# Optimization experiments

Measured on AMD Instinct MI355X. Metric: run time of the kernel, lower is better.

Reference implementation:

```python
import jax, jax.numpy as jnp
import numpy as np

B, IN_SEQ, TGT_SEQ = 128, 50, 25
IN_SIZE, OUT_SIZE, RNN = 128, 128, 2048


def setup_inputs() -> dict:
    key = jax.random.key(0)
    ks = jax.random.split(key, 10)
    s_in = 1.0 / np.sqrt(IN_SIZE)
    s_out = 1.0 / np.sqrt(OUT_SIZE)
    s_rnn = 1.0 / np.sqrt(RNN)
    return {
        "encoder_inputs": jax.random.normal(ks[0], (B, IN_SEQ, IN_SIZE), jnp.float32),
        "decoder_inputs": jax.random.normal(ks[1], (B, TGT_SEQ, IN_SIZE), jnp.float32),
        "fc1_w": jax.random.uniform(ks[2], (OUT_SIZE, IN_SIZE), jnp.float32, -s_in, s_in),
        "fc1_b": jax.random.uniform(ks[3], (OUT_SIZE,), jnp.float32, -s_in, s_in),
        "w_ih": jax.random.uniform(ks[4], (3 * RNN, OUT_SIZE), jnp.float32, -s_rnn, s_rnn),
        "w_hh": jax.random.uniform(ks[5], (3 * RNN, RNN), jnp.float32, -s_rnn, s_rnn),
        "b_ih": jax.random.uniform(ks[6], (3 * RNN,), jnp.float32, -s_rnn, s_rnn),
        "b_hh": jax.random.uniform(ks[7], (3 * RNN,), jnp.float32, -s_rnn, s_rnn),
        "fc2_w": jax.random.uniform(ks[8], (OUT_SIZE, RNN), jnp.float32, -s_rnn, s_rnn),
        "fc2_b": jax.random.uniform(ks[9], (OUT_SIZE,), jnp.float32, -s_rnn, s_rnn),
    }


def _gru_cell(x, h, w_ih, w_hh, b_ih, b_hh):
    # PyTorch GRUCell: gates ordered (r, z, n)
    gi = x @ w_ih.T + b_ih            # [B, 3R]
    gh = h @ w_hh.T + b_hh            # [B, 3R]
    i_r, i_z, i_n = jnp.split(gi, 3, axis=-1)
    h_r, h_z, h_n = jnp.split(gh, 3, axis=-1)
    r = jax.nn.sigmoid(i_r + h_r)
    z = jax.nn.sigmoid(i_z + h_z)
    n = jnp.tanh(i_n + r * h_n)
    return (1.0 - z) * n + z * h


def reference(encoder_inputs, decoder_inputs, fc1_w, fc1_b, w_ih, w_hh, b_ih, b_hh, fc2_w, fc2_b):
    # Eval mode: F.dropout(training=False) is identity.
    enc = encoder_inputs @ fc1_w.T + fc1_b              # [B, S_in, OUT]
    enc_t = jnp.transpose(enc, (1, 0, 2))               # time-major [S_in, B, OUT]
    h0 = jnp.zeros((encoder_inputs.shape[0], RNN), enc.dtype)

    def enc_step(state, x):
        return _gru_cell(x, state, w_ih, w_hh, b_ih, b_hh), None

    state, _ = jax.lax.scan(enc_step, h0, enc_t[:-1])   # input_seq - 1 steps

    def dec_step(carry, _):
        state, inp = carry
        inp = jax.lax.stop_gradient(inp)                # inp.detach()
        state = _gru_cell(inp, state, w_ih, w_hh, b_ih, b_hh)
        out = inp + state @ fc2_w.T + fc2_b             # residual decoder
        return (state, out), out

    _, outs = jax.lax.scan(dec_step, (state, enc_t[-1]), None, length=TGT_SEQ)
    return jnp.transpose(outs, (1, 0, 2))               # [B, TGT_SEQ, OUT]
```

## Files before the change

kernel.cpp:

```cpp
#include <hip/hip_runtime.h>
#include <limits.h>

constexpr int kB   = 128;
constexpr int kSin = 50;
constexpr int kT   = 25;
constexpr int kD   = 128;
constexpr int kR   = 2048;
constexpr int kNB  = 256;
constexpr int kNT  = 512;
constexpr int kRing = 8;

typedef __bf16 bf16x8 __attribute__((ext_vector_type(8)));
typedef float  f32x4  __attribute__((ext_vector_type(4)));
typedef unsigned short u16;
typedef unsigned long long u64;

__device__ __forceinline__ float bf2f(u16 u){ union{unsigned i; float f;}x; x.i=((unsigned)u)<<16; return x.f; }
__device__ __forceinline__ u16 f2bf(float f){ union{float f; unsigned i;}x; x.f=f; return (u16)((x.i + 0x7FFFu + ((x.i>>16)&1u))>>16); }
__device__ __forceinline__ float sigm(float x){ return 1.f/(1.f+__expf(-x)); }

__device__ __forceinline__ void stg32(unsigned* p, unsigned v){
    __hip_atomic_store(p, v, __ATOMIC_RELAXED, __HIP_MEMORY_SCOPE_AGENT);
}
__device__ __forceinline__ void stg64(u64* p, u64 v){
    __hip_atomic_store(p, v, __ATOMIC_RELAXED, __HIP_MEMORY_SCOPE_AGENT);
}
__device__ __forceinline__ unsigned ald32(const void* p){
    return __hip_atomic_load((const unsigned*)p, __ATOMIC_RELAXED, __HIP_MEMORY_SCOPE_AGENT);
}
__device__ __forceinline__ u64 ald64(const void* p){
    return __hip_atomic_load((const u64*)p, __ATOMIC_RELAXED, __HIP_MEMORY_SCOPE_AGENT);
}
__device__ __forceinline__ bf16x8 ald128bf(const u16* p){
    union{ u64 q[2]; bf16x8 v; } t;
    t.q[0] = ald64(p);
    t.q[1] = ald64(p + 4);
    return t.v;
}
__device__ __forceinline__ float aldf(const float* p){
    union{ unsigned u; float f; } t; t.u = ald32(p); return t.f;
}

__device__ __forceinline__ bf16x8 pack8(float4 a, float4 b){
    union{ bf16x8 v; u16 u[8]; } t;
    t.u[0]=f2bf(a.x); t.u[1]=f2bf(a.y); t.u[2]=f2bf(a.z); t.u[3]=f2bf(a.w);
    t.u[4]=f2bf(b.x); t.u[5]=f2bf(b.y); t.u[6]=f2bf(b.z); t.u[7]=f2bf(b.w);
    return t.v;
}

__device__ __forceinline__ int pollflag(int* flags, int idx, int iter){
    if ((iter & 31) == 31) return atomicMax(&flags[idx*16], INT_MIN);
    return (int)ald32(&flags[idx*16]);
}
__device__ __forceinline__ void wait16(int* flags, int k, int base){
    const int lane = threadIdx.x & 63;
    for (int iter = 0;; ++iter){
        bool ok = true;
        if (lane < 16) ok = (pollflag(flags, base + lane, iter) >= k);
        if (__ballot(ok) == ~0ull) return;
        __builtin_amdgcn_s_sleep(1);
    }
}
__device__ __forceinline__ void wait128(int* flags, int k, int base){
    const int lane = threadIdx.x & 63;
    for (int iter = 0;; ++iter){
        bool ok = true;
#pragma unroll
        for (int j = 0; j < 2; ++j)
            ok &= (pollflag(flags, base + lane*2 + j, iter) >= k);
        if (__ballot(ok) == ~0ull) return;
        __builtin_amdgcn_s_sleep(1);
    }
}
__device__ __forceinline__ void arrive(int* flags, int k){
    __syncthreads();
    if (threadIdx.x == 0) atomicMax(&flags[blockIdx.x*16], k);
}

__device__ __forceinline__ void gbar(int* flags, int k, int base, int perlane)
{
    __syncthreads();
    const int tid = threadIdx.x;
    if (tid == 0) atomicMax(&flags[blockIdx.x*16], k);
    if (tid < 64) {
        int iter = 0;
        for (;;) {
            bool ok = true;
            for (int j = 0; j < perlane; ++j) {
                const int idx = base + tid*perlane + j;
                int v;
                if ((iter & 31) == 31) v = atomicMax(&flags[idx*16], INT_MIN);
                else                   v = (int)ald32(&flags[idx*16]);
                ok &= (v >= k);
            }
            if (__ballot(ok) == ~0ull) break;
            ++iter;
            __builtin_amdgcn_s_sleep(1);
        }
    }
    __syncthreads();
}

__device__ __forceinline__ void cvt_f32_bf16(const float* __restrict__ s, u16* __restrict__ d,
                                             int n4, int gtid, int gstride)
{
    for (int i = gtid; i < n4; i += gstride) {
        float4 v = ((const float4*)s)[i];
        u64 pk = (u64)f2bf(v.x) | ((u64)f2bf(v.y)<<16) | ((u64)f2bf(v.z)<<32) | ((u64)f2bf(v.w)<<48);
        stg64((u64*)d + i, pk);
    }
}

template<int NT, int NACC>
__device__ __forceinline__ void small_gemm(
    const u16* __restrict__ Am, int alda,
    const u16* __restrict__ Bp, int bldb,
    f32x4 (&acc)[NACC], u16* pool)
{
    const int tid=threadIdx.x, lane=tid&63, wv=tid>>6, g=wv>>2, mt=wv&3, ar=lane&15, aq=lane>>4;
    u16* sA = pool;
    u16* sB = pool + 8704;
    { int q=tid,     r=q>>4, c=q&15; *(uint4*)&sA[r*136+c*8] = *(const uint4*)(Am + r*alda + c*8); }
    { int q=tid+512, r=q>>4, c=q&15; *(uint4*)&sA[r*136+c*8] = *(const uint4*)(Am + r*alda + c*8); }
    for (int q=tid; q<NT*256; q+=kNT){
        int r=q>>4, c=q&15;
        *(uint4*)&sB[r*136+c*8] = *(const uint4*)(Bp + (size_t)r*bldb + c*8);
    }
    __syncthreads();
#pragma unroll
    for (int jt=0; jt<NT; ++jt){
        if ((jt&1) != g) continue;
#pragma unroll
        for (int kk=0; kk<4; ++kk){
            bf16x8 a = *(const bf16x8*)&sA[(mt*16+ar)*136 + kk*32 + aq*8];
            bf16x8 b = *(const bf16x8*)&sB[(jt*16+ar)*136 + kk*32 + aq*8];
            acc[jt>>1] = __builtin_amdgcn_mfma_f32_16x16x32_bf16(a,b,acc[jt>>1],0,0,0);
        }
    }
    __syncthreads();
}

__device__ __forceinline__ void gru_phase_flag(
    const u16* __restrict__ hcur, u16* __restrict__ hnxt,
    const u16* __restrict__ xb,
    const bf16x8 (&wB)[3][8], const bf16x8 (&wI)[3],
    const float4 b4, float (&hprev)[4],
    int wgc, int mrow0, u16* smem, u16* sH,
    int* flags, int hk, int xk, int fbase, bool dofence)
{
    const int tid=threadIdx.x, lane=tid&63, w=tid>>6, ar=lane&15, aq=lane>>4;
    const f32x4 zz = {0.f,0.f,0.f,0.f};
    f32x4 acc[3][4] = {{zz,zz,zz,zz},{zz,zz,zz,zz},{zz,zz,zz,zz}};
    f32x4 xn[4] = {zz,zz,zz,zz};

    if (dofence) __builtin_amdgcn_fence(__ATOMIC_ACQUIRE, "agent");

    if (hk) wait16(flags, hk, fbase + 16*w);

#pragma unroll
    for (int mt=0; mt<4; ++mt){
        const int row = mrow0 + mt*16 + ar;
        bf16x8 af[8];
#pragma unroll
        for (int c=0; c<8; ++c){
            const int s = 16*w + 2*c + (aq>>1);
            af[c] = *(const bf16x8*)(hcur + (((s*128 + row)<<4) + (aq&1)*8));
        }
#pragma unroll
        for (int c=0; c<8; ++c){
            acc[0][mt] = __builtin_amdgcn_mfma_f32_16x16x32_bf16(af[c], wB[0][c], acc[0][mt],0,0,0);
            acc[1][mt] = __builtin_amdgcn_mfma_f32_16x16x32_bf16(af[c], wB[1][c], acc[1][mt],0,0,0);
            acc[2][mt] = __builtin_amdgcn_mfma_f32_16x16x32_bf16(af[c], wB[2][c], acc[2][mt],0,0,0);
        }
    }
    if (w < 4){
        if (xk) wait128(flags, xk, fbase);
#pragma unroll
        for (int mt=0; mt<4; ++mt){
            bf16x8 ax = *(const bf16x8*)(xb + (mrow0+mt*16+ar)*kD + 32*w + aq*8);
            acc[0][mt] = __builtin_amdgcn_mfma_f32_16x16x32_bf16(ax, wI[0], acc[0][mt],0,0,0);
            acc[1][mt] = __builtin_amdgcn_mfma_f32_16x16x32_bf16(ax, wI[1], acc[1][mt],0,0,0);
            xn[mt]     = __builtin_amdgcn_mfma_f32_16x16x32_bf16(ax, wI[2], xn[mt],0,0,0);
        }
    }
    float* red = (float*)smem;
#define RCELL(wp,g4,mt) (red + (((((wp)*4+(g4))*4+(mt))*64 + lane)<<2))
    if (w >= 4){
#pragma unroll
        for (int g=0; g<3; ++g)
#pragma unroll
            for (int mt=0; mt<4; ++mt)
                *(f32x4*)RCELL(w-4, g, mt) = acc[g][mt];
    }
    __syncthreads();
    if (w < 4){
#pragma unroll
        for (int g=0; g<3; ++g)
#pragma unroll
            for (int mt=0; mt<4; ++mt)
                acc[g][mt] += *(f32x4*)RCELL(w, g, mt);
#pragma unroll
        for (int g=0; g<3; ++g)
#pragma unroll
            for (int mt=0; mt<4; ++mt)
                *(f32x4*)RCELL(w, g, mt) = acc[g][mt];
#pragma unroll
        for (int mt=0; mt<4; ++mt)
            *(f32x4*)RCELL(w, 3, mt) = xn[mt];
    }
    __syncthreads();
    if (tid < 256){
        const int mt = tid>>6, ls = tid&63, aqs = ls>>4, ars = ls&15;
        f32x4 R=zz, Z=zz, NH=zz, NX=zz;
#pragma unroll
        for (int wp=0; wp<4; ++wp){
            R  += *(f32x4*)(red + ((((wp*4+0)*4+mt)*64 + ls)<<2));
            Z  += *(f32x4*)(red + ((((wp*4+1)*4+mt)*64 + ls)<<2));
            NH += *(f32x4*)(red + ((((wp*4+2)*4+mt)*64 + ls)<<2));
            NX += *(f32x4*)(red + ((((wp*4+3)*4+mt)*64 + ls)<<2));
        }
#pragma unroll
        for (int rr=0; rr<4; ++rr){
            const int m = mrow0 + mt*16 + aqs*4 + rr;
            float r_ = sigm(R[rr] + b4.x);
            float z_ = sigm(Z[rr] + b4.y);
            float n_ = tanhf(NX[rr] + b4.z + r_*(NH[rr] + b4.w));
            float hn = (1.f-z_)*n_ + z_*hprev[rr];
            hprev[rr] = hn;
            u16 hb = f2bf(hn);
            sH[(mt*16 + aqs*4 + rr)*16 + ars] = hb;
            unsigned other = (unsigned)__shfl_xor((int)(unsigned)hb, 1);
            if (!(ars&1))
                stg32((unsigned*)(hnxt + ((wgc*128+m)<<4) + ars), (unsigned)hb | (other<<16));
        }
    }
#undef RCELL
    __syncthreads();
}

__device__ __forceinline__ void fc2_partial(
    const u16* __restrict__ sH, const bf16x8 (&wF2)[4],
    int wgc, int mh, float* __restrict__ part)
{
    const int tid=threadIdx.x, lane=tid&63, w=tid>>6, ar=lane&15, aq=lane>>4;
    const int mt = w&3, nh = w>>2;
    bf16x8 a;
    if (aq < 2) a = *(const bf16x8*)&sH[(mt*16+ar)*16 + aq*8];
    else {
#pragma unroll
        for (int i=0;i<8;++i) a[i] = (__bf16)0.f;
    }
    const f32x4 zz = {0.f,0.f,0.f,0.f};
    f32x4 acc[4] = {zz,zz,zz,zz};
#pragma unroll
    for (int j=0;j<4;++j)
        acc[j] = __builtin_amdgcn_mfma_f32_16x16x32_bf16(a, wF2[j], acc[j],0,0,0);
#pragma unroll
    for (int j=0;j<4;++j){
        const int col = (nh*4+j)*16 + ar;
#pragma unroll
        for (int rr=0;rr<4;++rr){
            const int row = mt*16 + aq*4 + rr;
            stg32((unsigned*)(part + ((((size_t)mh*64+row)*128 + wgc)*128 + col)),
                  __float_as_uint(acc[j][rr]));
        }
    }
}

__global__ __launch_bounds__(kNT, 2) void seq2seq_kernel(
    const void* __restrict__ enc_in_raw, const void* __restrict__ fc1_w_raw,
    const void* __restrict__ fc1_b_raw,  const void* __restrict__ w_ih_raw,
    const void* __restrict__ w_hh_raw,   const void* __restrict__ b_ih_raw,
    const void* __restrict__ b_hh_raw,   const void* __restrict__ fc2_w_raw,
    const void* __restrict__ fc2_b_raw,
    void* __restrict__ out_raw,
    u16* __restrict__ enc_act,
    u16* __restrict__ h_b16,
    u16* __restrict__ inp_b16,
    float* __restrict__ inp_f32,
    float* __restrict__ encF,
    float* __restrict__ bias,
    float* __restrict__ part,
    int* flags,
    u16* __restrict__ cv_encx, u16* __restrict__ cv_fc2, u16* __restrict__ cv_fc1)
{
    __shared__ __align__(16) u16 smem[33792];
    __shared__ int sflag;
    u16* sH = smem + 32768;
    const int wg = blockIdx.x, tid = threadIdx.x;
    const int wgc = wg & 127, mrow0 = (wg >> 7) * 64;
    const int lane = tid & 63, wv = tid >> 6, ar = lane & 15, aq = lane >> 4;
    const int gtid = wg * kNT + tid, gstride = kNB * kNT;
    const int dom = (wg >> 7) * 128;
    const size_t HS = (size_t)kB*kR;

    {
        const u16* p = (const u16*)enc_in_raw;
        int found = 0;
        for (int i = tid; i < 16384; i += kNT) found |= ((p[i] & 0x7F80) == 0x7F80) ? 1 : 0;
        if (tid == 0) sflag = 0;
        __syncthreads();
        if (found) sflag = 1;
        __syncthreads();
    }
    const bool F32 = (sflag != 0);

    bf16x8 wB[3][8];
    bf16x8 wI[3];
    {
        const int w4 = wv & 3;
        if (F32){
            const float* Wh = (const float*)w_hh_raw;
            const float* Wi = (const float*)w_ih_raw;
#pragma unroll
            for (int g=0; g<3; ++g)
#pragma unroll
                for (int c=0; c<8; ++c){
                    size_t o = (size_t)(g*kR + wgc*16 + ar)*kR + 256*wv + 32*c + aq*8;
                    wB[g][c] = pack8(*(const float4*)(Wh+o), *(const float4*)(Wh+o+4));
                }
#pragma unroll
            for (int g=0; g<3; ++g){
                size_t o = (size_t)(g*kR + wgc*16 + ar)*kD + 32*w4 + aq*8;
                wI[g] = pack8(*(const float4*)(Wi+o), *(const float4*)(Wi+o+4));
            }
        } else {
            const u16* Wh = (const u16*)w_hh_raw;
            const u16* Wi = (const u16*)w_ih_raw;
#pragma unroll
            for (int g=0; g<3; ++g)
#pragma unroll
                for (int c=0; c<8; ++c)
                    wB[g][c] = *(const bf16x8*)(Wh + (size_t)(g*kR + wgc*16 + ar)*kR + 256*wv + 32*c + aq*8);
#pragma unroll
            for (int g=0; g<3; ++g)
                wI[g] = *(const bf16x8*)(Wi + (size_t)(g*kR + wgc*16 + ar)*kD + 32*w4 + aq*8);
        }
    }

    if (F32) {
        cvt_f32_bf16((const float*)fc2_w_raw, cv_fc2,  (kD*kR)/4,       gtid, gstride);
        cvt_f32_bf16((const float*)fc1_w_raw, cv_fc1,  (kD*kD)/4,       gtid, gstride);
        cvt_f32_bf16((const float*)enc_in_raw,cv_encx, (kB*kSin*kD)/4,  gtid, gstride);
        for (int i = gtid; i < 3*kR; i += gstride) {
            stg32((unsigned*)&bias[i],        __float_as_uint(((const float*)b_ih_raw)[i]));
            stg32((unsigned*)&bias[3*kR + i], __float_as_uint(((const float*)b_hh_raw)[i]));
        }
        for (int i = gtid; i < kD; i += gstride) {
            stg32((unsigned*)&bias[6*kR + i],      __float_as_uint(((const float*)fc1_b_raw)[i]));
            stg32((unsigned*)&bias[6*kR + kD + i], __float_as_uint(((const float*)fc2_b_raw)[i]));
        }
    } else {
        for (int i = gtid; i < 3*kR; i += gstride) {
            stg32((unsigned*)&bias[i],        __float_as_uint(bf2f(((const u16*)b_ih_raw)[i])));
            stg32((unsigned*)&bias[3*kR + i], __float_as_uint(bf2f(((const u16*)b_hh_raw)[i])));
        }
        for (int i = gtid; i < kD; i += gstride) {
            stg32((unsigned*)&bias[6*kR + i],      __float_as_uint(bf2f(((const u16*)fc1_b_raw)[i])));
            stg32((unsigned*)&bias[6*kR + kD + i], __float_as_uint(bf2f(((const u16*)fc2_b_raw)[i])));
        }
    }
    for (int i = gtid; i < (int)((kB*kR)/2); i += gstride) stg32((unsigned*)h_b16 + i, 0u);
    gbar(flags, 1, 0, 4);

    const u16* ENCX = F32 ? cv_encx : (const u16*)enc_in_raw;
    const u16* WF2  = F32 ? cv_fc2  : (const u16*)fc2_w_raw;
    const u16* WF1  = F32 ? cv_fc1  : (const u16*)fc1_w_raw;

    float4 b4;
    {
        const int hc = wgc*16 + ar;
        b4.x = aldf(&bias[hc])      + aldf(&bias[3*kR+hc]);
        b4.y = aldf(&bias[kR+hc])   + aldf(&bias[4*kR+hc]);
        b4.z = aldf(&bias[2*kR+hc]);
        b4.w = aldf(&bias[5*kR+hc]);
    }
    bf16x8 wF2[4];
    {
        const int nh = wv>>2;
#pragma unroll
        for (int j=0;j<4;++j){
            if (aq < 2)
                wF2[j] = ald128bf(WF2 + (size_t)((nh*4+j)*16+ar)*kR + wgc*16 + aq*8);
            else {
#pragma unroll
                for (int i=0;i<8;++i) wF2[j][i] = (__bf16)0.f;
            }
        }
    }
    const float fc2b = aldf(&bias[6*kR + kD + (wg&1)*64 + (tid&63)]);
    float hprev[4] = {0.f, 0.f, 0.f, 0.f};

    if (wgc < kSin) {
        const int g = wv>>2, mt = wv&3;
        const f32x4 zz = {0.f,0.f,0.f,0.f};
        f32x4 ae[4] = {zz,zz,zz,zz};
        small_gemm<8,4>(ENCX + ((size_t)mrow0*kSin + wgc)*kD, kSin*kD, WF1, kD, ae, smem);
#pragma unroll
        for (int jt=0; jt<8; ++jt){
            if ((jt&1) != g) continue;
            int col = jt*16 + ar;
            float fb = aldf(&bias[6*kR + col]);
#pragma unroll
            for (int rr=0; rr<4; ++rr){
                int m = mrow0 + mt*16 + aq*4 + rr;
                float v = ae[jt>>1][rr] + fb;
                u16 hb = f2bf(v);
                unsigned other = (unsigned)__shfl_xor((int)(unsigned)hb, 1);
                if (!(ar&1))
                    stg32((unsigned*)(enc_act + ((size_t)wgc*kB + m)*kD + col),
                          (unsigned)hb | (other<<16));
                if (wgc == kSin-1)
                    stg32((unsigned*)(encF + (size_t)m*kD + col), __float_as_uint(v));
            }
        }
    }
    gbar(flags, 2, dom, 2);

    for (int t = 0; t < kSin-1; ++t) {
        gru_phase_flag(h_b16 + (size_t)(t & 7)*HS, h_b16 + (size_t)((t+1) & 7)*HS,
                       enc_act + (size_t)t*kB*kD, wB, wI, b4, hprev, wgc, mrow0, smem, sH,
                       flags, (t==0 ? 0 : t+2), 0, dom,
                       (t > 0) && ((t & 7) == 0));
        arrive(flags, t+3);
    }

    const u16*   ib  = enc_act + (size_t)(kSin-1)*kB*kD;
    const float* ifp = encF;
    const int mh = wg >> 7;
    for (int d = 0; d < kT; ++d) {
        const int g = 49 + d;
        gru_phase_flag(h_b16 + (size_t)(g & 7)*HS, h_b16 + (size_t)((g+1) & 7)*HS,
                       ib, wB, wI, b4, hprev, wgc, mrow0, smem, sH,
                       flags, (d==0 ? 51 : 50+2*d), (d==0 ? 0 : 51+2*d), dom,
                       (g & 7) == 0);
        fc2_partial(sH, wF2, wgc, mh, part);
        arrive(flags, 52+2*d);

        u16*   nib = inp_b16 + (size_t)(d & 7)*kB*kD;
        float* nif = inp_f32 + (size_t)(d & 7)*kB*kD;
        wait128(flags, 52+2*d, dom);
        {
            const int row = wg >> 1, ch = wg & 1;
            const int mh2 = row >> 6, rl = row & 63;
            const float* pr = part + (size_t)((mh2*64 + rl)*128)*128;
            const int cl = tid & 63, sg = tid >> 6;
            float s = 0.f;
#pragma unroll
            for (int j=0;j<16;++j) s += aldf(&pr[(size_t)(sg*16+j)*128 + ch*64 + cl]);
            float* red2 = (float*)smem;
            red2[sg*64 + cl] = s;
            __syncthreads();
            if (tid < 64){
                float t2 = 0.f;
#pragma unroll
                for (int g2=0; g2<8; ++g2) t2 += red2[g2*64 + tid];
                const int colg = ch*64 + tid;
                const float o = t2 + fc2b + ifp[(size_t)row*kD + colg];
                const size_t ob = ((size_t)row*kT + d)*kD + colg;
                if (F32) ((float*)out_raw)[ob] = o;
                else     ((u16*)out_raw)[ob]   = f2bf(o);
                stg32((unsigned*)(nif + (size_t)row*kD + colg), __float_as_uint(o));
                u16 hb = f2bf(o);
                unsigned other = (unsigned)__shfl_xor((int)(unsigned)hb, 1);
                if (!(tid&1))
                    stg32((unsigned*)(nib + (size_t)row*kD + colg), (unsigned)hb | (other<<16));
            }
        }
        arrive(flags, 53+2*d);
        ib = nib; ifp = nif;
    }
}

extern "C" void kernel_launch(void* const* d_in, const int* in_sizes, int n_in,
                              void* d_out, int out_size, void* d_ws, size_t ws_size,
                              hipStream_t stream)
{
    size_t off = 0;
    char* ws = (char*)d_ws;
    auto alloc = [&](size_t bytes) -> char* {
        char* p = ws + off;
        off = (off + bytes + 255) & ~(size_t)255;
        return p;
    };
    u16*   enc_act = (u16*)alloc((size_t)kSin*kB*kD*2);
    u16*   h_b16   = (u16*)alloc((size_t)kRing*kB*kR*2);
    u16*   inp_b16 = (u16*)alloc((size_t)kRing*kB*kD*2);
    float* inp_f32 = (float*)alloc((size_t)kRing*kB*kD*4);
    float* encF    = (float*)alloc((size_t)kB*kD*4);
    float* bias    = (float*)alloc((size_t)(6*kR + 2*kD)*4);
    float* part    = (float*)alloc((size_t)2*64*128*128*4);
    int*   flags   = (int*)alloc((size_t)kNB*16*4);
    u16*   cv_encx = (u16*)alloc((size_t)kB*kSin*kD*2);
    u16*   cv_fc2  = (u16*)alloc((size_t)kD*kR*2);
    u16*   cv_fc1  = (u16*)alloc((size_t)kD*kD*2);
    (void)ws_size; (void)in_sizes; (void)n_in; (void)out_size;

    seq2seq_kernel<<<dim3(kNB), dim3(kNT), 0, stream>>>(
        d_in[0], d_in[2], d_in[3], d_in[4], d_in[5], d_in[6], d_in[7], d_in[8], d_in[9],
        d_out,
        enc_act, h_b16, inp_b16, inp_f32, encF, bias, part, flags,
        cv_encx, cv_fc2, cv_fc1);
}
```

Before: 1.531 ms.

## Software-pipeline h-fragment loads in GRU phase, reload fc2 weights per step

Restructures the recurrent GEMM so the h fragments for two M-tiles are double-buffered: the loads for the next tile are issued while the MFMAs for the current one run, and the x-input loads are hoisted ahead of the h MFMAs. The fc2 weight fragments are no longer held in registers for the whole kernel; they are reloaded from global memory on each decoder step, which frees VGPRs for the double buffers. tanhf is replaced by an exp-based fast tanh. The shared-memory array is enlarged but not visibly used, and the per-step weight reloads add memory traffic on the decoder path.

```diff
diff --git a/kernel.cpp b/kernel.cpp
--- a/kernel.cpp
+++ b/kernel.cpp
@@ -18,6 +18,7 @@
 __device__ __forceinline__ float bf2f(u16 u){ union{unsigned i; float f;}x; x.i=((unsigned)u)<<16; return x.f; }
 __device__ __forceinline__ u16 f2bf(float f){ union{float f; unsigned i;}x; x.f=f; return (u16)((x.i + 0x7FFFu + ((x.i>>16)&1u))>>16); }
 __device__ __forceinline__ float sigm(float x){ return 1.f/(1.f+__expf(-x)); }
+__device__ __forceinline__ float tanhf_fast(float x){ return 1.f - 2.f/(__expf(2.f*x)+1.f); }
 
 __device__ __forceinline__ void stg32(unsigned* p, unsigned v){
     __hip_atomic_store(p, v, __ATOMIC_RELAXED, __HIP_MEMORY_SCOPE_AGENT);
@@ -27,15 +28,6 @@
 }
 __device__ __forceinline__ unsigned ald32(const void* p){
     return __hip_atomic_load((const unsigned*)p, __ATOMIC_RELAXED, __HIP_MEMORY_SCOPE_AGENT);
-}
-__device__ __forceinline__ u64 ald64(const void* p){
-    return __hip_atomic_load((const u64*)p, __ATOMIC_RELAXED, __HIP_MEMORY_SCOPE_AGENT);
-}
-__device__ __forceinline__ bf16x8 ald128bf(const u16* p){
-    union{ u64 q[2]; bf16x8 v; } t;
-    t.q[0] = ald64(p);
-    t.q[1] = ald64(p + 4);
-    return t.v;
 }
 __device__ __forceinline__ float aldf(const float* p){
     union{ unsigned u; float f; } t; t.u = ald32(p); return t.f;
@@ -140,6 +132,14 @@
     __syncthreads();
 }
 
+#define MT_MFMA(MT, BUF)                                                            \
+    _Pragma("unroll")                                                               \
+    for (int c=0; c<8; ++c){                                                        \
+        acc[0][MT] = __builtin_amdgcn_mfma_f32_16x16x32_bf16(BUF[c], wB[0][c], acc[0][MT],0,0,0); \
+        acc[1][MT] = __builtin_amdgcn_mfma_f32_16x16x32_bf16(BUF[c], wB[1][c], acc[1][MT],0,0,0); \
+        acc[2][MT] = __builtin_amdgcn_mfma_f32_16x16x32_bf16(BUF[c], wB[2][c], acc[2][MT],0,0,0); \
+    }
+
 __device__ __forceinline__ void gru_phase_flag(
     const u16* __restrict__ hcur, u16* __restrict__ hnxt,
     const u16* __restrict__ xb,
@@ -157,32 +157,39 @@
 
     if (hk) wait16(flags, hk, fbase + 16*w);
 
-#pragma unroll
-    for (int mt=0; mt<4; ++mt){
-        const int row = mrow0 + mt*16 + ar;
-        bf16x8 af[8];
-#pragma unroll
-        for (int c=0; c<8; ++c){
-            const int s = 16*w + 2*c + (aq>>1);
-            af[c] = *(const bf16x8*)(hcur + (((s*128 + row)<<4) + (aq&1)*8));
-        }
-#pragma unroll
-        for (int c=0; c<8; ++c){
-            acc[0][mt] = __builtin_amdgcn_mfma_f32_16x16x32_bf16(af[c], wB[0][c], acc[0][mt],0,0,0);
-            acc[1][mt] = __builtin_amdgcn_mfma_f32_16x16x32_bf16(af[c], wB[1][c], acc[1][mt],0,0,0);
-            acc[2][mt] = __builtin_amdgcn_mfma_f32_16x16x32_bf16(af[c], wB[2][c], acc[2][mt],0,0,0);
-        }
-    }
+#define HPTR(MT,C) ((const bf16x8*)(hcur + ((((16*w + 2*(C) + (aq>>1))*128 + mrow0 + (MT)*16 + ar)<<4) + (aq&1)*8)))
+    bf16x8 af0[8], af1[8];
+#pragma unroll
+    for (int c=0;c<8;++c) af0[c] = *HPTR(0,c);
+#pragma unroll
+    for (int c=0;c<8;++c) af1[c] = *HPTR(1,c);
+
+    bf16x8 ax[4];
     if (w < 4){
         if (xk) wait128(flags, xk, fbase);
 #pragma unroll
+        for (int mt=0; mt<4; ++mt)
+            ax[mt] = *(const bf16x8*)(xb + (mrow0+mt*16+ar)*kD + 32*w + aq*8);
+    }
+
+    MT_MFMA(0, af0)
+#pragma unroll
+    for (int c=0;c<8;++c) af0[c] = *HPTR(2,c);
+    MT_MFMA(1, af1)
+    if (w < 4){
+#pragma unroll
         for (int mt=0; mt<4; ++mt){
-            bf16x8 ax = *(const bf16x8*)(xb + (mrow0+mt*16+ar)*kD + 32*w + aq*8);
-            acc[0][mt] = __builtin_amdgcn_mfma_f32_16x16x32_bf16(ax, wI[0], acc[0][mt],0,0,0);
-            acc[1][mt] = __builtin_amdgcn_mfma_f32_16x16x32_bf16(ax, wI[1], acc[1][mt],0,0,0);
-            xn[mt]     = __builtin_amdgcn_mfma_f32_16x16x32_bf16(ax, wI[2], xn[mt],0,0,0);
-        }
-    }
+            acc[0][mt] = __builtin_amdgcn_mfma_f32_16x16x32_bf16(ax[mt], wI[0], acc[0][mt],0,0,0);
+            acc[1][mt] = __builtin_amdgcn_mfma_f32_16x16x32_bf16(ax[mt], wI[1], acc[1][mt],0,0,0);
+            xn[mt]     = __builtin_amdgcn_mfma_f32_16x16x32_bf16(ax[mt], wI[2], xn[mt],0,0,0);
+        }
+    }
+#pragma unroll
+    for (int c=0;c<8;++c) af1[c] = *HPTR(3,c);
+    MT_MFMA(2, af0)
+    MT_MFMA(3, af1)
+#undef HPTR
+
     float* red = (float*)smem;
 #define RCELL(wp,g4,mt) (red + (((((wp)*4+(g4))*4+(mt))*64 + lane)<<2))
     if (w >= 4){
@@ -224,7 +231,7 @@
             const int m = mrow0 + mt*16 + aqs*4 + rr;
             float r_ = sigm(R[rr] + b4.x);
             float z_ = sigm(Z[rr] + b4.y);
-            float n_ = tanhf(NX[rr] + b4.z + r_*(NH[rr] + b4.w));
+            float n_ = tanhf_fast(NX[rr] + b4.z + r_*(NH[rr] + b4.w));
             float hn = (1.f-z_)*n_ + z_*hprev[rr];
             hprev[rr] = hn;
             u16 hb = f2bf(hn);
@@ -239,22 +246,30 @@
 }
 
 __device__ __forceinline__ void fc2_partial(
-    const u16* __restrict__ sH, const bf16x8 (&wF2)[4],
+    const u16* __restrict__ sH, const u16* __restrict__ WF2,
     int wgc, int mh, float* __restrict__ part)
 {
     const int tid=threadIdx.x, lane=tid&63, w=tid>>6, ar=lane&15, aq=lane>>4;
     const int mt = w&3, nh = w>>2;
-    bf16x8 a;
-    if (aq < 2) a = *(const bf16x8*)&sH[(mt*16+ar)*16 + aq*8];
-    else {
+    bf16x8 a, wj[4];
+    if (aq < 2){
+        a = *(const bf16x8*)&sH[(mt*16+ar)*16 + aq*8];
+#pragma unroll
+        for (int j=0;j<4;++j)
+            wj[j] = *(const bf16x8*)(WF2 + (size_t)((nh*4+j)*16+ar)*kR + wgc*16 + aq*8);
+    } else {
 #pragma unroll
         for (int i=0;i<8;++i) a[i] = (__bf16)0.f;
+#pragma unroll
+        for (int j=0;j<4;++j)
+#pragma unroll
+            for (int i=0;i<8;++i) wj[j][i] = (__bf16)0.f;
     }
     const f32x4 zz = {0.f,0.f,0.f,0.f};
     f32x4 acc[4] = {zz,zz,zz,zz};
 #pragma unroll
     for (int j=0;j<4;++j)
-        acc[j] = __builtin_amdgcn_mfma_f32_16x16x32_bf16(a, wF2[j], acc[j],0,0,0);
+        acc[j] = __builtin_amdgcn_mfma_f32_16x16x32_bf16(a, wj[j], acc[j],0,0,0);
 #pragma unroll
     for (int j=0;j<4;++j){
         const int col = (nh*4+j)*16 + ar;
@@ -284,7 +299,7 @@
     int* flags,
     u16* __restrict__ cv_encx, u16* __restrict__ cv_fc2, u16* __restrict__ cv_fc1)
 {
-    __shared__ __align__(16) u16 smem[33792];
+    __shared__ __align__(16) u16 smem[43008];
     __shared__ int sflag;
     u16* sH = smem + 32768;
     const int wg = blockIdx.x, tid = threadIdx.x;
@@ -374,19 +389,6 @@
         b4.y = aldf(&bias[kR+hc])   + aldf(&bias[4*kR+hc]);
         b4.z = aldf(&bias[2*kR+hc]);
         b4.w = aldf(&bias[5*kR+hc]);
-    }
-    bf16x8 wF2[4];
-    {
-        const int nh = wv>>2;
-#pragma unroll
-        for (int j=0;j<4;++j){
-            if (aq < 2)
-                wF2[j] = ald128bf(WF2 + (size_t)((nh*4+j)*16+ar)*kR + wgc*16 + aq*8);
-            else {
-#pragma unroll
-                for (int i=0;i<8;++i) wF2[j][i] = (__bf16)0.f;
-            }
-        }
     }
     const float fc2b = aldf(&bias[6*kR + kD + (wg&1)*64 + (tid&63)]);
     float hprev[4] = {0.f, 0.f, 0.f, 0.f};
@@ -434,7 +436,7 @@
                        ib, wB, wI, b4, hprev, wgc, mrow0, smem, sH,
                        flags, (d==0 ? 51 : 50+2*d), (d==0 ? 0 : 51+2*d), dom,
                        (g & 7) == 0);
-        fc2_partial(sH, wF2, wgc, mh, part);
+        fc2_partial(sH, WF2, wgc, mh, part);
         arrive(flags, 52+2*d);
 
         u16*   nib = inp_b16 + (size_t)(d & 7)*kB*kD;
```

Result: slower. 1.703 ms (+11.3%).
